# Kernel tuning notes

Hardware: AMD Instinct MI355X
Metric: run time of the kernel (lower is better)

Reference implementation:

```python
import jax, jax.numpy as jnp
import numpy as np

UNITS, N, S = 256, 64, 4
BATCH, T = 64, 1024


def setup_inputs() -> dict:
    key = jax.random.key(0)
    k0, k1, k2, k3 = jax.random.split(key, 4)
    return {
        "inputs": jax.random.uniform(k0, (BATCH, T, S), dtype=jnp.float32),
        "transition_kernel": jax.random.normal(k1, (UNITS, N, N), dtype=jnp.float32),
        "emission_kernel": jax.random.normal(k2, (UNITS, N, S), dtype=jnp.float32),
        "init_kernel": jax.random.normal(k3, (UNITS, N), dtype=jnp.float32),
    }


def reference(inputs, transition_kernel, emission_kernel, init_kernel):
    # Softmaxed HMM parameters (computed once; the TF cell recomputes per step).
    A = jax.nn.softmax(transition_kernel, axis=-1)  # [U, N, N] transitions
    B = jax.nn.softmax(emission_kernel, axis=-1)    # [U, N, S] emissions
    I = jax.nn.softmax(init_kernel, axis=-1)        # [U, N]    initial dist

    batch = inputs.shape[0]
    U, Nn = init_kernel.shape

    alpha0 = jnp.zeros((batch, U, Nn), dtype=inputs.dtype)
    ll0 = jnp.zeros((batch, U), dtype=inputs.dtype)
    is_init0 = jnp.ones((batch,), dtype=inputs.dtype)  # HMM starts in init at t=0

    def step(carry, x_t):
        alpha, ll, is_init = carry
        # R[b,u,j] = is_init[b]*I[u,j] + sum_i A[u,i,j]*alpha[b,u,i]  (A^T matvec)
        R = is_init[:, None, None] * I[None] + jnp.einsum("uij,bui->buj", A, alpha)
        # E[b,u,i] = sum_c B[u,i,c] * x_t[b,c]
        E = jnp.einsum("unc,bc->bun", B, x_t)
        fwd = E * R                              # [B, U, N]
        Ssum = jnp.sum(fwd, axis=-1)             # [B, U]
        ll = ll + jnp.log(Ssum)
        alpha = fwd / Ssum[..., None]            # normalized forward variable
        return (alpha, ll, jnp.zeros_like(is_init)), ll

    xs = jnp.swapaxes(inputs, 0, 1)  # [T, B, S]
    (_, _, _), lls = jax.lax.scan(step, (alpha0, ll0, is_init0), xs)
    # whole-sequence output: cumulative log-likelihood per step, [B, T, U]
    return jnp.swapaxes(lls, 0, 1)
```

## Files before the change

### kernel.cpp

```cpp
#include <hip/hip_runtime.h>


#define U_ 256
#define N_ 64
#define S_ 4
#define B_ 64
#define T_ 1024
#define ROWP 72

typedef __attribute__((ext_vector_type(8))) __bf16 bf16x8;
typedef __attribute__((ext_vector_type(4))) float floatx4;

__device__ __forceinline__ int sig(int jt, int m) {
    return 32 * (jt >> 1) + 4 * (jt & 1) + 8 * (m >> 2) + (m & 3);
}

__launch_bounds__(256, 1)
__global__ void hmm_fwd_kernel(const float* __restrict__ xg,
                               const float* __restrict__ trans,
                               const float* __restrict__ emis,
                               const float* __restrict__ initk,
                               float* __restrict__ out)
{
    __shared__ __bf16 AT[N_ * ROWP];
    __shared__ float BemS[N_][S_];
    __shared__ float IS[N_];

    const int bid = blockIdx.x;
    const int u = ((bid & 7) << 5) | (bid >> 3);
    const int tid = threadIdx.x;
    const int lane = tid & 63;
    const int w = tid >> 6;
    const int q = lane >> 4;
    const int l = lane & 15;

    if (tid < 64) {
        const float* rowp = trans + (u * N_ + tid) * N_;
        float v[N_];
        #pragma unroll
        for (int k = 0; k < 16; ++k) {
            floatx4 t4 = *(const floatx4*)(rowp + 4 * k);
            v[4*k] = t4.x; v[4*k+1] = t4.y; v[4*k+2] = t4.z; v[4*k+3] = t4.w;
        }
        float m = v[0];
        #pragma unroll
        for (int j = 1; j < N_; ++j) m = fmaxf(m, v[j]);
        float s = 0.f;
        #pragma unroll
        for (int j = 0; j < N_; ++j) { v[j] = __expf(v[j] - m); s += v[j]; }
        float inv = 1.0f / s;
        #pragma unroll
        for (int j = 0; j < N_; ++j) AT[j * ROWP + tid] = (__bf16)(v[j] * inv);
    } else if (tid < 128) {
        int n = tid - 64;
        floatx4 e4 = *(const floatx4*)(emis + (u * N_ + n) * S_);
        float m = fmaxf(fmaxf(e4.x, e4.y), fmaxf(e4.z, e4.w));
        float a = __expf(e4.x - m), b2 = __expf(e4.y - m);
        float c = __expf(e4.z - m), d = __expf(e4.w - m);
        float inv = 1.0f / (a + b2 + c + d);
        BemS[n][0] = a*inv; BemS[n][1] = b2*inv; BemS[n][2] = c*inv; BemS[n][3] = d*inv;
    } else if (tid < 192) {
        int j = tid - 128;
        float v = initk[u * N_ + j];
        float m = v;
        #pragma unroll
        for (int s = 1; s < 64; s <<= 1) m = fmaxf(m, __shfl_xor(m, s, 64));
        float e = __expf(v - m);
        float ssum = e;
        #pragma unroll
        for (int s = 1; s < 64; s <<= 1) ssum += __shfl_xor(ssum, s, 64);
        IS[j] = e / ssum;
    }
    __syncthreads();

    bf16x8 afrag[4][2];
    #pragma unroll
    for (int jt = 0; jt < 4; ++jt)
        #pragma unroll
        for (int kt = 0; kt < 2; ++kt)
            afrag[jt][kt] = *(const bf16x8*)&AT[sig(jt, l) * ROWP + 32*kt + 8*q];

    bf16x8 afragE[4];
    #pragma unroll
    for (int jt = 0; jt < 4; ++jt) {
        #pragma unroll
        for (int p = 0; p < 8; ++p) afragE[jt][p] = (__bf16)0.f;
        if (q == 0) {
            #pragma unroll
            for (int c = 0; c < 4; ++c)
                afragE[jt][c] = (__bf16)BemS[sig(jt, l)][c];
        }
    }

    floatx4 Rv[4];
    #pragma unroll
    for (int jt = 0; jt < 4; ++jt)
        #pragma unroll
        for (int r = 0; r < 4; ++r) Rv[jt][r] = IS[sig(jt, 4*q + r)];

    __asm__ volatile("" ::: "memory");

    const int b = 16*w + l;
    const float* xin = xg + b * (T_ * S_);
    float* llout = out + (size_t)b * T_ * U_ + u;

    const floatx4 z = {0.f, 0.f, 0.f, 0.f};
    floatx4 Ev[4];
    float ll = 0.f, sp1 = 0.f, sp2 = 0.f, rsA = 1.0f;

    bf16x8 be;
    #pragma unroll
    for (int p = 0; p < 8; ++p) be[p] = (__bf16)0.f;

    floatx4 x0 = *(const floatx4*)xin;
    floatx4 xvA[4], xvB[4];
    #pragma unroll
    for (int i = 0; i < 4; ++i)
        xvA[i] = *(const floatx4*)(xin + (1 + i) * S_);

    {
        be[0] = (__bf16)x0.x; be[1] = (__bf16)x0.y;
        be[2] = (__bf16)x0.z; be[3] = (__bf16)x0.w;
        #pragma unroll
        for (int jt = 0; jt < 4; ++jt)
            Ev[jt] = __builtin_amdgcn_mfma_f32_16x16x32_bf16(afragE[jt], be, z, 0, 0, 0);
    }

    float hist[8];
    bool own = false;

    auto step = [&](const floatx4& xsrc, int slot) {
        floatx4 gv[4];
        #pragma unroll
        for (int jt = 0; jt < 4; ++jt) gv[jt] = Ev[jt] * Rv[jt];

        bf16x8 bf0, bf1;
        #pragma unroll
        for (int p = 0; p < 4; ++p) {
            bf0[p]     = (__bf16)gv[0][p];
            bf0[4 + p] = (__bf16)gv[1][p];
            bf1[p]     = (__bf16)gv[2][p];
            bf1[4 + p] = (__bf16)gv[3][p];
        }

        #pragma unroll
        for (int jt = 0; jt < 4; ++jt) {
            floatx4 acc = __builtin_amdgcn_mfma_f32_16x16x32_bf16(afrag[jt][0], bf0, z, 0, 0, 0);
            Rv[jt] = __builtin_amdgcn_mfma_f32_16x16x32_bf16(afrag[jt][1], bf1, acc, 0, 0, 0);
        }

        floatx4 s4 = (gv[0] + gv[1]) + (gv[2] + gv[3]);
        float p0 = (s4.x + s4.y) + (s4.z + s4.w);
        float a16 = __shfl_xor(p0, 16, 64);
        float a32 = __shfl_xor(p0, 32, 64);
        float a48 = __shfl_xor(p0, 48, 64);
        float ss = (p0 + a16) + (a32 + a48);
        float sg = __logf(ss);
        float rs = __builtin_amdgcn_rcpf(ss);

        ll += sg - sp1 + sp2;
        sp2 = sp1; sp1 = sg;
        hist[slot] = own ? ll : hist[slot];

        floatx4 xs = xsrc * rsA;
        be[0] = (__bf16)xs.x; be[1] = (__bf16)xs.y;
        be[2] = (__bf16)xs.z; be[3] = (__bf16)xs.w;
        #pragma unroll
        for (int jt = 0; jt < 4; ++jt)
            Ev[jt] = __builtin_amdgcn_mfma_f32_16x16x32_bf16(afragE[jt], be, z, 0, 0, 0);
        rsA = rs;
    };

    for (int tb = 0; tb < T_; tb += 8) {
        own = (q == ((tb >> 3) & 3));

        #pragma unroll
        for (int i = 0; i < 4; ++i) {
            int ti = tb + 5 + i; ti = (ti < T_) ? ti : T_ - 1;
            xvB[i] = *(const floatx4*)(xin + ti * S_);
        }

        step(xvA[0], 0); step(xvA[1], 1); step(xvA[2], 2); step(xvA[3], 3);

        #pragma unroll
        for (int i = 0; i < 4; ++i) {
            int ti = tb + 9 + i; ti = (ti < T_) ? ti : T_ - 1;
            xvA[i] = *(const floatx4*)(xin + ti * S_);
        }

        step(xvB[0], 4); step(xvB[1], 5); step(xvB[2], 6); step(xvB[3], 7);

        if ((tb & 24) == 24) {
            float* fp = llout + (size_t)((tb - 24) + 8 * q) * U_;
            #pragma unroll
            for (int k = 0; k < 8; ++k) fp[(size_t)k * U_] = hist[k];
        }
    }
}

extern "C" void kernel_launch(void* const* d_in, const int* in_sizes, int n_in,
                              void* d_out, int out_size, void* d_ws, size_t ws_size,
                              hipStream_t stream) {
    const float* xg    = (const float*)d_in[0];
    const float* trans = (const float*)d_in[1];
    const float* emis  = (const float*)d_in[2];
    const float* initk = (const float*)d_in[3];
    float* out = (float*)d_out;
    hipLaunchKernelGGL(hmm_fwd_kernel, dim3(U_), dim3(256), 0, stream,
                       xg, trans, emis, initk, out);
}
```

Baseline: 371.3 us.

## Defer per-step log and sum reduction off the recurrence critical path

New measurement: 362.0 us. 1.03x faster.

```diff
diff --git a/kernel.cpp b/kernel.cpp
--- a/kernel.cpp
+++ b/kernel.cpp
@@ -106,7 +106,7 @@
 
     const floatx4 z = {0.f, 0.f, 0.f, 0.f};
     floatx4 Ev[4];
-    float ll = 0.f, sp1 = 0.f, sp2 = 0.f, rsA = 1.0f;
+    float rsA = 1.0f;
 
     bf16x8 be;
     #pragma unroll
@@ -127,7 +127,16 @@
     }
 
     float hist[8];
-    bool own = false;
+    float e1 = 1.0f, pe1 = 1.0f, Cacc = 0.f;
+    bool own = false, ownN = false;
+    float pp0, pa16, pa32, pa48;
+
+    auto consume = [&](int kprev) {
+        float ss = (pp0 + pa16) + (pa32 + pa48);
+        rsA = __builtin_amdgcn_rcpf(ss);
+        hist[kprev] = own ? ss : hist[kprev];
+        if (kprev == 7) e1 = ownN ? ss : e1;
+    };
 
     auto step = [&](const floatx4& xsrc, int slot) {
         floatx4 gv[4];
@@ -149,18 +158,7 @@
             Rv[jt] = __builtin_amdgcn_mfma_f32_16x16x32_bf16(afrag[jt][1], bf1, acc, 0, 0, 0);
         }
 
-        floatx4 s4 = (gv[0] + gv[1]) + (gv[2] + gv[3]);
-        float p0 = (s4.x + s4.y) + (s4.z + s4.w);
-        float a16 = __shfl_xor(p0, 16, 64);
-        float a32 = __shfl_xor(p0, 32, 64);
-        float a48 = __shfl_xor(p0, 48, 64);
-        float ss = (p0 + a16) + (a32 + a48);
-        float sg = __logf(ss);
-        float rs = __builtin_amdgcn_rcpf(ss);
-
-        ll += sg - sp1 + sp2;
-        sp2 = sp1; sp1 = sg;
-        hist[slot] = own ? ll : hist[slot];
+        if (slot > 0) consume(slot - 1);
 
         floatx4 xs = xsrc * rsA;
         be[0] = (__bf16)xs.x; be[1] = (__bf16)xs.y;
@@ -168,11 +166,19 @@
         #pragma unroll
         for (int jt = 0; jt < 4; ++jt)
             Ev[jt] = __builtin_amdgcn_mfma_f32_16x16x32_bf16(afragE[jt], be, z, 0, 0, 0);
-        rsA = rs;
+
+        floatx4 s4 = (gv[0] + gv[1]) + (gv[2] + gv[3]);
+        pp0  = (s4.x + s4.y) + (s4.z + s4.w);
+        pa16 = __shfl_xor(pp0, 16, 64);
+        pa32 = __shfl_xor(pp0, 32, 64);
+        pa48 = __shfl_xor(pp0, 48, 64);
     };
 
     for (int tb = 0; tb < T_; tb += 8) {
-        own = (q == ((tb >> 3) & 3));
+        const int oct = (tb >> 3) & 3;
+        own  = (q == oct);
+        ownN = (q == ((oct + 1) & 3));
+        if ((tb & 24) == 0) pe1 = e1;
 
         #pragma unroll
         for (int i = 0; i < 4; ++i) {
@@ -190,10 +196,31 @@
 
         step(xvB[0], 4); step(xvB[1], 5); step(xvB[2], 6); step(xvB[3], 7);
 
+        consume(7);
+
         if ((tb & 24) == 24) {
-            float* fp = llout + (size_t)((tb - 24) + 8 * q) * U_;
-            #pragma unroll
-            for (int k = 0; k < 8; ++k) fp[(size_t)k * U_] = hist[k];
+            const int tb0 = tb - 24;
+            float sg[8], P[8];
+            #pragma unroll
+            for (int k = 0; k < 8; ++k) sg[k] = __logf(hist[k]);
+            P[0] = sg[0];
+            #pragma unroll
+            for (int k = 1; k < 8; ++k) P[k] = P[k-1] + sg[k];
+            float Loc = P[7];
+            float a  = __shfl_xor(Loc, 16, 64);
+            float b2 = __shfl_xor(Loc, 32, 64);
+            float c  = __shfl_xor(Loc, 48, 64);
+            float bc = b2 + c;
+            float off = ((q & 1) ? a : 0.f) + ((q & 2) ? bc : 0.f);
+            float base = Cacc + off;
+            float se1 = __logf((q == 0) ? pe1 : e1);
+            float* fp = llout + (size_t)(tb0 + 8 * q) * U_;
+            fp[0]          = sg[0] + base - se1;
+            fp[U_]         = sg[1] + base;
+            #pragma unroll
+            for (int k = 2; k < 8; ++k)
+                fp[(size_t)k * U_] = sg[k] + base + P[k-2];
+            Cacc += Loc + a + bc;
         }
     }
 }
```
